# Kernel optimization log

Measured on AMD Instinct MI355X. Metric: run time of the kernel, lower is better.

The kernel has to match this reference:

```python
import jax, jax.numpy as jnp
import numpy as np

EPS = 1e-8
TEMPERATURE = 1.0


def setup_inputs() -> dict:
    key = jax.random.key(0)
    basin_seq = jax.random.normal(key, (4, 512, 64), dtype=jnp.float32)
    residual_scale = jnp.ones((), dtype=jnp.float32)  # nn.Parameter(torch.tensor(1.0))
    return {"basin_seq": basin_seq, "residual_scale": residual_scale}


def _project_to_simplex(x):
    sp = jax.nn.softplus(x)
    p = sp / (sp.sum(axis=-1, keepdims=True) + EPS)
    return jnp.maximum(p, EPS)


def _qfi_attention_weights(x, temperature):
    # x: (B, T, D)
    p = _project_to_simplex(x)
    # fisher_rao_distance_simplex re-normalizes both operands
    p = p / (p.sum(axis=-1, keepdims=True) + EPS)
    # Faithful: eps is inside the sqrt, so this is a true (B,T,T,D) reduction,
    # not sqrt(p) @ sqrt(p)^T.
    inner = jnp.sqrt(p[:, :, None, :] * p[:, None, :, :] + EPS).sum(axis=-1)  # (B,T,T)
    inner = jnp.clip(inner, -1.0 + 1e-6, 1.0 - 1e-6)
    dist = 2.0 * jnp.arccos(inner)
    logits = -dist / max(float(temperature), 1e-6)
    return jax.nn.softmax(logits, axis=-1)  # (B,T,T)


def _phi_from_activations(acts):
    # acts: (B, T, D)
    t = acts.shape[1]
    x = acts - acts.mean(axis=1, keepdims=True)
    cov = jnp.einsum('btd,bte->bde', x, x) / (t + EPS)
    var = jnp.maximum(jnp.diagonal(cov, axis1=-2, axis2=-1), EPS)  # (B,D)
    denom = jnp.maximum(jnp.sqrt(var[:, :, None] * var[:, None, :]), EPS)
    corr = jnp.clip(cov / denom, -1.0, 1.0)
    d = corr.shape[-1]
    offdiag = corr * (1.0 - jnp.eye(d, dtype=corr.dtype))
    return jnp.abs(offdiag).mean(axis=(-2, -1))  # (B,)


def _kappa_proxy(x):
    return jnp.linalg.norm(x, axis=-1).mean(axis=-1)  # (B,)


def reference(basin_seq, residual_scale):
    x = basin_seq
    for _ in range(2):
        w = _qfi_attention_weights(x, TEMPERATURE)
        x_attn = jnp.einsum('bij,bjd->bid', w, x)
        x = 0.5 * x + 0.5 * x_attn
        x = x + 0.01 * residual_scale * (x_attn - x)
    phi = _phi_from_activations(x)
    kappa = _kappa_proxy(x)
    return (x, phi, kappa)
```

## Files before the change

kernel.cpp:

```cpp
#include <hip/hip_runtime.h>
#include <math.h>

#define B_ 4
#define T_ 512
#define D_ 64
#define EPS 1e-8f

__device__ __forceinline__ float wave_sum(float v) {
#pragma unroll
  for (int m = 1; m < 64; m <<= 1) v += __shfl_xor(v, m, 64);
  return v;
}
__device__ __forceinline__ float softplus_f(float x) {
  return fmaxf(x, 0.0f) + log1pf(expf(-fabsf(x)));
}

#define DOT4(ACC, A, Bv) \
  ACC = fmaf((A).x, (Bv).x, fmaf((A).y, (Bv).y, fmaf((A).z, (Bv).z, fmaf((A).w, (Bv).w, ACC))))

__global__ __launch_bounds__(256) void proj_kernel(const float* __restrict__ x,
                                                   float* __restrict__ s) {
  int wave = threadIdx.x >> 6, lane = threadIdx.x & 63;
  int row = blockIdx.x * 4 + wave;
  float sp = softplus_f(x[row * D_ + lane]);
  float s1 = wave_sum(sp);
  float p = sp / (s1 + EPS);
  p = fmaxf(p, EPS);
  float s2 = wave_sum(p);
  s[row * D_ + lane] = sqrtf(p / (s2 + EPS));
}

__device__ __forceinline__ void stage512(const float* __restrict__ g,
                                         float* __restrict__ lds, int tid) {
#pragma unroll
  for (int h = 0; h < 2; ++h) {
    float4 v[8];
#pragma unroll
    for (int r = 0; r < 8; ++r) {
      int slot = (h * 8 + r) * 512 + tid;
      int j = slot >> 4, c4 = slot & 15;
      v[r] = *(const float4*)(g + j * 64 + ((c4 ^ ((j >> 2) & 7)) << 2));
    }
#pragma unroll
    for (int r = 0; r < 8; ++r) {
      int slot = (h * 8 + r) * 512 + tid;
      int j = slot >> 4, c4 = slot & 15;
      *(float4*)(lds + j * 64 + (c4 << 2)) = v[r];
    }
  }
}

__global__ __launch_bounds__(512) void fiter_kernel(const float* __restrict__ s_g,
                                                    const float* __restrict__ x_g,
                                                    const float* __restrict__ rsp,
                                                    float* __restrict__ xout,
                                                    float* __restrict__ sout) {
  int b = blockIdx.y, i0 = blockIdx.x * 8;
  int tid = threadIdx.x;
  int w = tid >> 6, lane = tid & 63;
  const float* sb = s_g + (size_t)b * (T_ * D_);
  const float* xb = x_g + (size_t)b * (T_ * D_);

  __shared__ __align__(16) float sx[512 * 64];
  __shared__ __align__(16) float wlds[8 * 516];
  __shared__ __align__(16) float redv[8 * 68];
  __shared__ float redM[8][8];
  __shared__ float redS[8][8];

  stage512(sb, sx, tid);
  __syncthreads();

  int i4 = lane >> 4, j16 = lane & 15;
  int ia0 = i0 + 2 * i4;
  const float* A0 = sx + ia0 * 64;
  const float* A1 = A0 + 64;
  int mA0 = (ia0 >> 2) & 7, mA1 = ((ia0 + 1) >> 2) & 7;
  const float* Bp = sx + (w * 64 + 4 * j16) * 64;
  int mB = j16 & 7;

  float acc[2][4];
#pragma unroll
  for (int r = 0; r < 2; ++r)
#pragma unroll
    for (int c = 0; c < 4; ++c) acc[r][c] = 0.f;

#pragma unroll
  for (int d4 = 0; d4 < 16; ++d4) {
    float4 a0 = *(const float4*)(A0 + ((d4 ^ mA0) << 2));
    float4 a1 = *(const float4*)(A1 + ((d4 ^ mA1) << 2));
    int ob = (d4 ^ mB) << 2;
    float4 b0 = *(const float4*)(Bp + ob);
    float4 b1 = *(const float4*)(Bp + 64 + ob);
    float4 b2 = *(const float4*)(Bp + 128 + ob);
    float4 b3 = *(const float4*)(Bp + 192 + ob);
    DOT4(acc[0][0], a0, b0); DOT4(acc[0][1], a0, b1);
    DOT4(acc[0][2], a0, b2); DOT4(acc[0][3], a0, b3);
    DOT4(acc[1][0], a1, b0); DOT4(acc[1][1], a1, b1);
    DOT4(acc[1][2], a1, b2); DOT4(acc[1][3], a1, b3);
  }

  float S[2][4];
#pragma unroll
  for (int r = 0; r < 2; ++r)
#pragma unroll
    for (int c = 0; c < 4; ++c) {
      float inner = fminf(fmaxf(acc[r][c], -1.0f + 1e-6f), 1.0f - 1e-6f);
      S[r][c] = -2.0f * acosf(inner);
    }

  float m0 = fmaxf(fmaxf(S[0][0], S[0][1]), fmaxf(S[0][2], S[0][3]));
  float m1 = fmaxf(fmaxf(S[1][0], S[1][1]), fmaxf(S[1][2], S[1][3]));
#pragma unroll
  for (int mm = 1; mm < 16; mm <<= 1) {
    m0 = fmaxf(m0, __shfl_xor(m0, mm, 64));
    m1 = fmaxf(m1, __shfl_xor(m1, mm, 64));
  }
  if (j16 == 0) { redM[2 * i4][w] = m0; redM[2 * i4 + 1][w] = m1; }
  __syncthreads();

  stage512(xb, sx, tid);

  float M0 = redM[2 * i4][0], M1 = redM[2 * i4 + 1][0];
#pragma unroll
  for (int q = 1; q < 8; ++q) {
    M0 = fmaxf(M0, redM[2 * i4][q]);
    M1 = fmaxf(M1, redM[2 * i4 + 1][q]);
  }
  float e[2][4];
  float sl0 = 0.f, sl1 = 0.f;
#pragma unroll
  for (int c = 0; c < 4; ++c) {
    e[0][c] = __expf(S[0][c] - M0); sl0 += e[0][c];
    e[1][c] = __expf(S[1][c] - M1); sl1 += e[1][c];
  }
#pragma unroll
  for (int mm = 1; mm < 16; mm <<= 1) {
    sl0 += __shfl_xor(sl0, mm, 64);
    sl1 += __shfl_xor(sl1, mm, 64);
  }
  if (j16 == 0) { redS[2 * i4][w] = sl0; redS[2 * i4 + 1][w] = sl1; }
  int wb = w * 64 + 4 * j16;
#pragma unroll
  for (int r = 0; r < 2; ++r)
#pragma unroll
    for (int c = 0; c < 4; ++c) wlds[(2 * i4 + r) * 516 + wb + c] = e[r][c];
  __syncthreads();

  int js = tid & 15, dg = (tid >> 4) & 15, ig = tid >> 8;
  int xcol = ((dg ^ (js & 7)) << 2);
  float pacc[4][4];
#pragma unroll
  for (int ii = 0; ii < 4; ++ii)
#pragma unroll
    for (int k = 0; k < 4; ++k) pacc[ii][k] = 0.f;

#pragma unroll 2
  for (int jj = 0; jj < 8; ++jj) {
    int jbase = jj * 64 + js * 4;
    const float* xr = sx + jbase * 64 + xcol;
    float4 x0 = *(const float4*)(xr);
    float4 x1 = *(const float4*)(xr + 64);
    float4 x2 = *(const float4*)(xr + 128);
    float4 x3 = *(const float4*)(xr + 192);
#pragma unroll
    for (int ii = 0; ii < 4; ++ii) {
      float4 wv = *(const float4*)(wlds + (4 * ig + ii) * 516 + jbase);
      pacc[ii][0] = fmaf(wv.x, x0.x, fmaf(wv.y, x1.x, fmaf(wv.z, x2.x, fmaf(wv.w, x3.x, pacc[ii][0]))));
      pacc[ii][1] = fmaf(wv.x, x0.y, fmaf(wv.y, x1.y, fmaf(wv.z, x2.y, fmaf(wv.w, x3.y, pacc[ii][1]))));
      pacc[ii][2] = fmaf(wv.x, x0.z, fmaf(wv.y, x1.z, fmaf(wv.z, x2.z, fmaf(wv.w, x3.z, pacc[ii][2]))));
      pacc[ii][3] = fmaf(wv.x, x0.w, fmaf(wv.y, x1.w, fmaf(wv.z, x2.w, fmaf(wv.w, x3.w, pacc[ii][3]))));
    }
  }
#pragma unroll
  for (int ii = 0; ii < 4; ++ii)
#pragma unroll
    for (int k = 0; k < 4; ++k) {
      float v = pacc[ii][k];
      v += __shfl_xor(v, 1, 64);
      v += __shfl_xor(v, 2, 64);
      v += __shfl_xor(v, 4, 64);
      v += __shfl_xor(v, 8, 64);
      pacc[ii][k] = v;
    }
  if (js == 0) {
#pragma unroll
    for (int ii = 0; ii < 4; ++ii)
      *(float4*)(redv + (4 * ig + ii) * 68 + (dg << 2)) =
          make_float4(pacc[ii][0], pacc[ii][1], pacc[ii][2], pacc[ii][3]);
  }
  __syncthreads();

  {
    int row = w, d = lane;
    float ssum = 0.f;
#pragma unroll
    for (int q = 0; q < 8; ++q) ssum += redS[row][q];
    float xa = redv[row * 68 + d] / ssum;
    int ir = i0 + row;
    int mr = (ir >> 2) & 7;
    float xv = sx[ir * 64 + (((d >> 2) ^ mr) << 2) + (d & 3)];
    float c01 = 0.01f * rsp[0];
    float xn = 0.5f * (1.0f - c01) * xv + 0.5f * (1.0f + c01) * xa;
    size_t gi = ((size_t)(b * T_) + ir) * D_ + d;
    xout[gi] = xn;
    float sp = softplus_f(xn);
    float s1 = wave_sum(sp);
    float p = sp / (s1 + EPS);
    p = fmaxf(p, EPS);
    float s2 = wave_sum(p);
    sout[gi] = sqrtf(p / (s2 + EPS));
  }
}

__global__ __launch_bounds__(256) void p1_kernel(const float* __restrict__ x,
                                                 float* __restrict__ covp,
                                                 float* __restrict__ meanp,
                                                 float* __restrict__ kappap) {
  int blk = blockIdx.x;
  int b = blk >> 5, sl = blk & 31;
  const float* xb = x + ((size_t)(b * T_) + sl * 16) * D_;
  __shared__ float tile[16][68];
  __shared__ float red2[4][64];
  __shared__ float kred[4];
  int tid = threadIdx.x;
  {
    int row = tid >> 4, c4 = tid & 15;
    *(float4*)&tile[row][c4 * 4] = *(const float4*)(xb + row * D_ + c4 * 4);
  }
  __syncthreads();

  {
    int tr = tid >> 4, qq = tid & 15;
    float ksq = 0.f;
#pragma unroll
    for (int k = 0; k < 4; ++k) {
      float v = tile[tr][qq * 4 + k];
      ksq = fmaf(v, v, ksq);
    }
    ksq += __shfl_xor(ksq, 1, 64);
    ksq += __shfl_xor(ksq, 2, 64);
    ksq += __shfl_xor(ksq, 4, 64);
    ksq += __shfl_xor(ksq, 8, 64);
    float contrib = (qq == 0) ? sqrtf(ksq) : 0.f;
    contrib = wave_sum(contrib);
    if ((tid & 63) == 0) kred[tid >> 6] = contrib;
  }

  {
    int d = tid & 63, q = tid >> 6;
    float ms = 0.f;
#pragma unroll
    for (int tt = 0; tt < 4; ++tt) ms += tile[q * 4 + tt][d];
    red2[q][d] = ms;
  }

  int dd = tid >> 2, e16 = tid & 3;
  float acc[16];
#pragma unroll
  for (int k = 0; k < 16; ++k) acc[k] = 0.f;
#pragma unroll
  for (int tt = 0; tt < 16; ++tt) {
    float xd = tile[tt][dd];
    const float4* te = (const float4*)&tile[tt][e16 * 16];
    float4 v0 = te[0], v1 = te[1], v2 = te[2], v3 = te[3];
    acc[0]  = fmaf(xd, v0.x, acc[0]);  acc[1]  = fmaf(xd, v0.y, acc[1]);
    acc[2]  = fmaf(xd, v0.z, acc[2]);  acc[3]  = fmaf(xd, v0.w, acc[3]);
    acc[4]  = fmaf(xd, v1.x, acc[4]);  acc[5]  = fmaf(xd, v1.y, acc[5]);
    acc[6]  = fmaf(xd, v1.z, acc[6]);  acc[7]  = fmaf(xd, v1.w, acc[7]);
    acc[8]  = fmaf(xd, v2.x, acc[8]);  acc[9]  = fmaf(xd, v2.y, acc[9]);
    acc[10] = fmaf(xd, v2.z, acc[10]); acc[11] = fmaf(xd, v2.w, acc[11]);
    acc[12] = fmaf(xd, v3.x, acc[12]); acc[13] = fmaf(xd, v3.y, acc[13]);
    acc[14] = fmaf(xd, v3.z, acc[14]); acc[15] = fmaf(xd, v3.w, acc[15]);
  }
  float* cp = covp + (size_t)blk * 4096 + dd * 64 + e16 * 16;
#pragma unroll
  for (int kk = 0; kk < 4; ++kk)
    *(float4*)(cp + kk * 4) =
        make_float4(acc[kk * 4], acc[kk * 4 + 1], acc[kk * 4 + 2], acc[kk * 4 + 3]);
  __syncthreads();
  if (tid < 64)
    meanp[blk * 64 + tid] = red2[0][tid] + red2[1][tid] + red2[2][tid] + red2[3][tid];
  if (tid == 0) kappap[blk] = kred[0] + kred[1] + kred[2] + kred[3];
}

__global__ __launch_bounds__(1024) void p2_kernel(const float* __restrict__ covp,
                                                  const float* __restrict__ meanp,
                                                  const float* __restrict__ kappap,
                                                  float* __restrict__ out) {
  int b = blockIdx.x;
  __shared__ float mu[64];
  __shared__ float var[64];
  __shared__ float phired[16];
  int tid = threadIdx.x;
  if (tid < 64) {
    float m = 0.f;
#pragma unroll
    for (int s = 0; s < 32; ++s) m += meanp[(b * 32 + s) * 64 + tid];
    mu[tid] = m * (1.0f / 512.0f);
  }
  __syncthreads();

  int dd = tid >> 4, e4 = tid & 15;
  float acc[4] = {0.f, 0.f, 0.f, 0.f};
#pragma unroll
  for (int s = 0; s < 32; ++s) {
    float4 v = *(const float4*)(covp + (size_t)(b * 32 + s) * 4096 + dd * 64 + e4 * 4);
    acc[0] += v.x; acc[1] += v.y; acc[2] += v.z; acc[3] += v.w;
  }
  float mud = mu[dd];
#pragma unroll
  for (int k = 0; k < 4; ++k)
    acc[k] = acc[k] * (1.0f / 512.0f) - mud * mu[e4 * 4 + k];
  if (e4 == (dd >> 2)) var[dd] = fmaxf(acc[dd & 3], EPS);
  __syncthreads();

  float vd = var[dd];
  float psum = 0.f;
#pragma unroll
  for (int k = 0; k < 4; ++k) {
    int e = e4 * 4 + k;
    if (e == dd) continue;
    float denom = fmaxf(sqrtf(vd * var[e]), EPS);
    float cc = fminf(fmaxf(acc[k] / denom, -1.0f), 1.0f);
    psum += fabsf(cc);
  }
  psum = wave_sum(psum);
  if ((tid & 63) == 0) phired[tid >> 6] = psum;
  __syncthreads();
  if (tid == 0) {
    float ph = 0.f;
#pragma unroll
    for (int q = 0; q < 16; ++q) ph += phired[q];
    out[B_ * T_ * D_ + b] = ph * (1.0f / 4096.0f);
    float ks = 0.f;
#pragma unroll
    for (int s = 0; s < 32; ++s) ks += kappap[b * 32 + s];
    out[B_ * T_ * D_ + B_ + b] = ks * (1.0f / 512.0f);
  }
}

extern "C" void kernel_launch(void* const* d_in, const int* in_sizes, int n_in,
                              void* d_out, int out_size, void* d_ws, size_t ws_size,
                              hipStream_t stream) {
  const float* x0 = (const float*)d_in[0];
  const float* rs = (const float*)d_in[1];
  float* out = (float*)d_out;
  float* s0    = (float*)d_ws;
  float* s1    = s0 + B_ * T_ * D_;
  float* x1    = s1 + B_ * T_ * D_;
  float* covp  = x1 + B_ * T_ * D_;
  float* meanp = covp + 128 * 4096;
  float* kappap = meanp + 128 * 64;

  dim3 fgrd(64, 4);
  proj_kernel<<<(B_ * T_) / 4, 256, 0, stream>>>(x0, s0);
  fiter_kernel<<<fgrd, 512, 0, stream>>>(s0, x0, rs, x1, s1);
  fiter_kernel<<<fgrd, 512, 0, stream>>>(s1, x1, rs, out, s0);
  p1_kernel<<<128, 256, 0, stream>>>(out, covp, meanp, kappap);
  p2_kernel<<<4, 1024, 0, stream>>>(covp, meanp, kappap, out);
}
```

Baseline: 96.12 us.

## Fuse simplex projection into attention kernel and merge stats kernels via last-block counter

Removes the standalone projection kernel. Each attention block now stages raw x into LDS and computes softplus-simplex-sqrt for all 512 rows of its batch in place, so the s buffers are neither written nor reread through global memory. The two covariance/phi kernels are merged into one: an atomic per-batch counter picks the last finishing block, which does the final reduction. This cuts launches from five to three, at the price of redundant transcendental work in every attention block plus threadfence/atomic overhead.

Result: slower. 173.9 us (+80.9%).

```diff
diff --git a/kernel.cpp b/kernel.cpp
--- a/kernel.cpp
+++ b/kernel.cpp
@@ -18,18 +18,6 @@
 #define DOT4(ACC, A, Bv) \
   ACC = fmaf((A).x, (Bv).x, fmaf((A).y, (Bv).y, fmaf((A).z, (Bv).z, fmaf((A).w, (Bv).w, ACC))))
 
-__global__ __launch_bounds__(256) void proj_kernel(const float* __restrict__ x,
-                                                   float* __restrict__ s) {
-  int wave = threadIdx.x >> 6, lane = threadIdx.x & 63;
-  int row = blockIdx.x * 4 + wave;
-  float sp = softplus_f(x[row * D_ + lane]);
-  float s1 = wave_sum(sp);
-  float p = sp / (s1 + EPS);
-  p = fmaxf(p, EPS);
-  float s2 = wave_sum(p);
-  s[row * D_ + lane] = sqrtf(p / (s2 + EPS));
-}
-
 __device__ __forceinline__ void stage512(const float* __restrict__ g,
                                          float* __restrict__ lds, int tid) {
 #pragma unroll
@@ -50,16 +38,17 @@
   }
 }
 
-__global__ __launch_bounds__(512) void fiter_kernel(const float* __restrict__ s_g,
-                                                    const float* __restrict__ x_g,
+template <int ZERO_CNT>
+__global__ __launch_bounds__(512) void fiter_kernel(const float* __restrict__ x_g,
                                                     const float* __restrict__ rsp,
                                                     float* __restrict__ xout,
-                                                    float* __restrict__ sout) {
+                                                    unsigned int* __restrict__ cnt) {
   int b = blockIdx.y, i0 = blockIdx.x * 8;
   int tid = threadIdx.x;
   int w = tid >> 6, lane = tid & 63;
-  const float* sb = s_g + (size_t)b * (T_ * D_);
   const float* xb = x_g + (size_t)b * (T_ * D_);
+
+  if (ZERO_CNT && blockIdx.x == 0 && blockIdx.y == 0 && tid < B_) cnt[tid] = 0u;
 
   __shared__ __align__(16) float sx[512 * 64];
   __shared__ __align__(16) float wlds[8 * 516];
@@ -67,7 +56,41 @@
   __shared__ float redM[8][8];
   __shared__ float redS[8][8];
 
-  stage512(sb, sx, tid);
+  stage512(xb, sx, tid);
+  __syncthreads();
+
+  {
+    int g = lane >> 4, d4 = lane & 15;
+#pragma unroll
+    for (int it = 0; it < 16; ++it) {
+      int r = (w << 6) + (it << 2) + g;
+      int mr = (r >> 2) & 7;
+      float* p4 = sx + r * 64 + ((d4 ^ mr) << 2);
+      float4 v = *(const float4*)p4;
+      float4 sp;
+      sp.x = softplus_f(v.x); sp.y = softplus_f(v.y);
+      sp.z = softplus_f(v.z); sp.w = softplus_f(v.w);
+      float loc = sp.x + sp.y + sp.z + sp.w;
+      loc += __shfl_xor(loc, 1, 64);
+      loc += __shfl_xor(loc, 2, 64);
+      loc += __shfl_xor(loc, 4, 64);
+      loc += __shfl_xor(loc, 8, 64);
+      float inv1 = 1.0f / (loc + EPS);
+      float4 p;
+      p.x = fmaxf(sp.x * inv1, EPS); p.y = fmaxf(sp.y * inv1, EPS);
+      p.z = fmaxf(sp.z * inv1, EPS); p.w = fmaxf(sp.w * inv1, EPS);
+      float loc2 = p.x + p.y + p.z + p.w;
+      loc2 += __shfl_xor(loc2, 1, 64);
+      loc2 += __shfl_xor(loc2, 2, 64);
+      loc2 += __shfl_xor(loc2, 4, 64);
+      loc2 += __shfl_xor(loc2, 8, 64);
+      float inv2 = 1.0f / (loc2 + EPS);
+      float4 sv;
+      sv.x = sqrtf(p.x * inv2); sv.y = sqrtf(p.y * inv2);
+      sv.z = sqrtf(p.z * inv2); sv.w = sqrtf(p.w * inv2);
+      *(float4*)p4 = sv;
+    }
+  }
   __syncthreads();
 
   int i4 = lane >> 4, j16 = lane & 15;
@@ -201,27 +224,23 @@
     float xv = sx[ir * 64 + (((d >> 2) ^ mr) << 2) + (d & 3)];
     float c01 = 0.01f * rsp[0];
     float xn = 0.5f * (1.0f - c01) * xv + 0.5f * (1.0f + c01) * xa;
-    size_t gi = ((size_t)(b * T_) + ir) * D_ + d;
-    xout[gi] = xn;
-    float sp = softplus_f(xn);
-    float s1 = wave_sum(sp);
-    float p = sp / (s1 + EPS);
-    p = fmaxf(p, EPS);
-    float s2 = wave_sum(p);
-    sout[gi] = sqrtf(p / (s2 + EPS));
-  }
-}
-
-__global__ __launch_bounds__(256) void p1_kernel(const float* __restrict__ x,
-                                                 float* __restrict__ covp,
-                                                 float* __restrict__ meanp,
-                                                 float* __restrict__ kappap) {
+    xout[((size_t)(b * T_) + ir) * D_ + d] = xn;
+  }
+}
+
+__global__ __launch_bounds__(256) void stats_kernel(const float* __restrict__ x,
+                                                    float* __restrict__ covp,
+                                                    float* __restrict__ meanp,
+                                                    float* __restrict__ kappap,
+                                                    unsigned int* __restrict__ cnt,
+                                                    float* __restrict__ out) {
   int blk = blockIdx.x;
-  int b = blk >> 5, sl = blk & 31;
-  const float* xb = x + ((size_t)(b * T_) + sl * 16) * D_;
+  int b = blk >> 5;
+  const float* xb = x + (size_t)blk * (16 * D_);
   __shared__ float tile[16][68];
   __shared__ float red2[4][64];
   __shared__ float kred[4];
+  __shared__ int lastflag;
   int tid = threadIdx.x;
   {
     int row = tid >> 4, c4 = tid & 15;
@@ -254,44 +273,49 @@
     red2[q][d] = ms;
   }
 
-  int dd = tid >> 2, e16 = tid & 3;
-  float acc[16];
-#pragma unroll
-  for (int k = 0; k < 16; ++k) acc[k] = 0.f;
-#pragma unroll
-  for (int tt = 0; tt < 16; ++tt) {
-    float xd = tile[tt][dd];
-    const float4* te = (const float4*)&tile[tt][e16 * 16];
-    float4 v0 = te[0], v1 = te[1], v2 = te[2], v3 = te[3];
-    acc[0]  = fmaf(xd, v0.x, acc[0]);  acc[1]  = fmaf(xd, v0.y, acc[1]);
-    acc[2]  = fmaf(xd, v0.z, acc[2]);  acc[3]  = fmaf(xd, v0.w, acc[3]);
-    acc[4]  = fmaf(xd, v1.x, acc[4]);  acc[5]  = fmaf(xd, v1.y, acc[5]);
-    acc[6]  = fmaf(xd, v1.z, acc[6]);  acc[7]  = fmaf(xd, v1.w, acc[7]);
-    acc[8]  = fmaf(xd, v2.x, acc[8]);  acc[9]  = fmaf(xd, v2.y, acc[9]);
-    acc[10] = fmaf(xd, v2.z, acc[10]); acc[11] = fmaf(xd, v2.w, acc[11]);
-    acc[12] = fmaf(xd, v3.x, acc[12]); acc[13] = fmaf(xd, v3.y, acc[13]);
-    acc[14] = fmaf(xd, v3.z, acc[14]); acc[15] = fmaf(xd, v3.w, acc[15]);
-  }
-  float* cp = covp + (size_t)blk * 4096 + dd * 64 + e16 * 16;
-#pragma unroll
-  for (int kk = 0; kk < 4; ++kk)
-    *(float4*)(cp + kk * 4) =
-        make_float4(acc[kk * 4], acc[kk * 4 + 1], acc[kk * 4 + 2], acc[kk * 4 + 3]);
+  {
+    int dd = tid >> 2, e16 = tid & 3;
+    float acc[16];
+#pragma unroll
+    for (int k = 0; k < 16; ++k) acc[k] = 0.f;
+#pragma unroll
+    for (int tt = 0; tt < 16; ++tt) {
+      float xd = tile[tt][dd];
+      const float4* te = (const float4*)&tile[tt][e16 * 16];
+      float4 v0 = te[0], v1 = te[1], v2 = te[2], v3 = te[3];
+      acc[0]  = fmaf(xd, v0.x, acc[0]);  acc[1]  = fmaf(xd, v0.y, acc[1]);
+      acc[2]  = fmaf(xd, v0.z, acc[2]);  acc[3]  = fmaf(xd, v0.w, acc[3]);
+      acc[4]  = fmaf(xd, v1.x, acc[4]);  acc[5]  = fmaf(xd, v1.y, acc[5]);
+      acc[6]  = fmaf(xd, v1.z, acc[6]);  acc[7]  = fmaf(xd, v1.w, acc[7]);
+      acc[8]  = fmaf(xd, v2.x, acc[8]);  acc[9]  = fmaf(xd, v2.y, acc[9]);
+      acc[10] = fmaf(xd, v2.z, acc[10]); acc[11] = fmaf(xd, v2.w, acc[11]);
+      acc[12] = fmaf(xd, v3.x, acc[12]); acc[13] = fmaf(xd, v3.y, acc[13]);
+      acc[14] = fmaf(xd, v3.z, acc[14]); acc[15] = fmaf(xd, v3.w, acc[15]);
+    }
+    float* cp = covp + (size_t)blk * 4096 + dd * 64 + e16 * 16;
+#pragma unroll
+    for (int kk = 0; kk < 4; ++kk)
+      *(float4*)(cp + kk * 4) =
+          make_float4(acc[kk * 4], acc[kk * 4 + 1], acc[kk * 4 + 2], acc[kk * 4 + 3]);
+  }
   __syncthreads();
   if (tid < 64)
     meanp[blk * 64 + tid] = red2[0][tid] + red2[1][tid] + red2[2][tid] + red2[3][tid];
   if (tid == 0) kappap[blk] = kred[0] + kred[1] + kred[2] + kred[3];
-}
-
-__global__ __launch_bounds__(1024) void p2_kernel(const float* __restrict__ covp,
-                                                  const float* __restrict__ meanp,
-                                                  const float* __restrict__ kappap,
-                                                  float* __restrict__ out) {
-  int b = blockIdx.x;
+
+  __threadfence();
+  __syncthreads();
+  if (tid == 0) {
+    unsigned int old = atomicAdd(&cnt[b], 1u);
+    lastflag = (old == 31u);
+  }
+  __syncthreads();
+  if (!lastflag) return;
+  __threadfence();
+
   __shared__ float mu[64];
   __shared__ float var[64];
-  __shared__ float phired[16];
-  int tid = threadIdx.x;
+  __shared__ float phired[4];
   if (tid < 64) {
     float m = 0.f;
 #pragma unroll
@@ -300,25 +324,32 @@
   }
   __syncthreads();
 
-  int dd = tid >> 4, e4 = tid & 15;
-  float acc[4] = {0.f, 0.f, 0.f, 0.f};
+  int dd = tid >> 2, e16 = tid & 3;
+  float acc[16];
+#pragma unroll
+  for (int k = 0; k < 16; ++k) acc[k] = 0.f;
 #pragma unroll
   for (int s = 0; s < 32; ++s) {
-    float4 v = *(const float4*)(covp + (size_t)(b * 32 + s) * 4096 + dd * 64 + e4 * 4);
-    acc[0] += v.x; acc[1] += v.y; acc[2] += v.z; acc[3] += v.w;
+    const float* cp = covp + (size_t)(b * 32 + s) * 4096 + dd * 64 + e16 * 16;
+#pragma unroll
+    for (int kk = 0; kk < 4; ++kk) {
+      float4 v = *(const float4*)(cp + kk * 4);
+      acc[kk * 4] += v.x; acc[kk * 4 + 1] += v.y;
+      acc[kk * 4 + 2] += v.z; acc[kk * 4 + 3] += v.w;
+    }
   }
   float mud = mu[dd];
 #pragma unroll
-  for (int k = 0; k < 4; ++k)
-    acc[k] = acc[k] * (1.0f / 512.0f) - mud * mu[e4 * 4 + k];
-  if (e4 == (dd >> 2)) var[dd] = fmaxf(acc[dd & 3], EPS);
+  for (int k = 0; k < 16; ++k)
+    acc[k] = acc[k] * (1.0f / 512.0f) - mud * mu[e16 * 16 + k];
+  if (e16 == (dd >> 4)) var[dd] = fmaxf(acc[dd & 15], EPS);
   __syncthreads();
 
   float vd = var[dd];
   float psum = 0.f;
 #pragma unroll
-  for (int k = 0; k < 4; ++k) {
-    int e = e4 * 4 + k;
+  for (int k = 0; k < 16; ++k) {
+    int e = e16 * 16 + k;
     if (e == dd) continue;
     float denom = fmaxf(sqrtf(vd * var[e]), EPS);
     float cc = fminf(fmaxf(acc[k] / denom, -1.0f), 1.0f);
@@ -328,10 +359,8 @@
   if ((tid & 63) == 0) phired[tid >> 6] = psum;
   __syncthreads();
   if (tid == 0) {
-    float ph = 0.f;
-#pragma unroll
-    for (int q = 0; q < 16; ++q) ph += phired[q];
-    out[B_ * T_ * D_ + b] = ph * (1.0f / 4096.0f);
+    out[B_ * T_ * D_ + b] = (phired[0] + phired[1] + phired[2] + phired[3]) *
+                            (1.0f / 4096.0f);
     float ks = 0.f;
 #pragma unroll
     for (int s = 0; s < 32; ++s) ks += kappap[b * 32 + s];
@@ -345,17 +374,14 @@
   const float* x0 = (const float*)d_in[0];
   const float* rs = (const float*)d_in[1];
   float* out = (float*)d_out;
-  float* s0    = (float*)d_ws;
-  float* s1    = s0 + B_ * T_ * D_;
-  float* x1    = s1 + B_ * T_ * D_;
+  float* x1    = (float*)d_ws;
   float* covp  = x1 + B_ * T_ * D_;
   float* meanp = covp + 128 * 4096;
   float* kappap = meanp + 128 * 64;
+  unsigned int* cnt = (unsigned int*)(kappap + 128);
 
   dim3 fgrd(64, 4);
-  proj_kernel<<<(B_ * T_) / 4, 256, 0, stream>>>(x0, s0);
-  fiter_kernel<<<fgrd, 512, 0, stream>>>(s0, x0, rs, x1, s1);
-  fiter_kernel<<<fgrd, 512, 0, stream>>>(s1, x1, rs, out, s0);
-  p1_kernel<<<128, 256, 0, stream>>>(out, covp, meanp, kappap);
-  p2_kernel<<<4, 1024, 0, stream>>>(covp, meanp, kappap, out);
-}
+  fiter_kernel<1><<<fgrd, 512, 0, stream>>>(x0, rs, x1, cnt);
+  fiter_kernel<0><<<fgrd, 512, 0, stream>>>(x1, rs, out, cnt);
+  stats_kernel<<<128, 256, 0, stream>>>(out, covp, meanp, kappap, cnt, out);
+}
```

## Fuse all five kernels into one cooperative kernel with grid syncs

Applied to the files above, without the earlier changes.

Merges the projection, both attention iterations, and the two covariance/phi/kappa reduction stages into a single cooperative launch of 256 blocks. Grid-wide syncs replace the kernel boundaries. This removes four launch gaps and their tail effects. In exchange, the final reduction stages run inside 512-thread blocks with only 128 or 4 active blocks, and every block still carries about 150KB of LDS, so occupancy stays at one block per CU. The second iteration also skips writing the unused simplex output.

Measured after the change: 209.0 us. +117.5%, slower.

```diff
diff --git a/kernel.cpp b/kernel.cpp
--- a/kernel.cpp
+++ b/kernel.cpp
@@ -1,5 +1,8 @@
 #include <hip/hip_runtime.h>
+#include <hip/hip_cooperative_groups.h>
 #include <math.h>
+
+namespace cg = cooperative_groups;
 
 #define B_ 4
 #define T_ 512
@@ -18,18 +21,6 @@
 #define DOT4(ACC, A, Bv) \
   ACC = fmaf((A).x, (Bv).x, fmaf((A).y, (Bv).y, fmaf((A).z, (Bv).z, fmaf((A).w, (Bv).w, ACC))))
 
-__global__ __launch_bounds__(256) void proj_kernel(const float* __restrict__ x,
-                                                   float* __restrict__ s) {
-  int wave = threadIdx.x >> 6, lane = threadIdx.x & 63;
-  int row = blockIdx.x * 4 + wave;
-  float sp = softplus_f(x[row * D_ + lane]);
-  float s1 = wave_sum(sp);
-  float p = sp / (s1 + EPS);
-  p = fmaxf(p, EPS);
-  float s2 = wave_sum(p);
-  s[row * D_ + lane] = sqrtf(p / (s2 + EPS));
-}
-
 __device__ __forceinline__ void stage512(const float* __restrict__ g,
                                          float* __restrict__ lds, int tid) {
 #pragma unroll
@@ -50,22 +41,13 @@
   }
 }
 
-__global__ __launch_bounds__(512) void fiter_kernel(const float* __restrict__ s_g,
-                                                    const float* __restrict__ x_g,
-                                                    const float* __restrict__ rsp,
-                                                    float* __restrict__ xout,
-                                                    float* __restrict__ sout) {
-  int b = blockIdx.y, i0 = blockIdx.x * 8;
-  int tid = threadIdx.x;
+__device__ __forceinline__ void fiter_body(
+    const float* __restrict__ sb, const float* __restrict__ xb,
+    float* __restrict__ xoutb, float* __restrict__ soutb, int i0, int tid,
+    float c01, float* __restrict__ sx, float* __restrict__ wlds,
+    float* __restrict__ redv, float* __restrict__ redM,
+    float* __restrict__ redS, int write_s) {
   int w = tid >> 6, lane = tid & 63;
-  const float* sb = s_g + (size_t)b * (T_ * D_);
-  const float* xb = x_g + (size_t)b * (T_ * D_);
-
-  __shared__ __align__(16) float sx[512 * 64];
-  __shared__ __align__(16) float wlds[8 * 516];
-  __shared__ __align__(16) float redv[8 * 68];
-  __shared__ float redM[8][8];
-  __shared__ float redS[8][8];
 
   stage512(sb, sx, tid);
   __syncthreads();
@@ -115,16 +97,16 @@
     m0 = fmaxf(m0, __shfl_xor(m0, mm, 64));
     m1 = fmaxf(m1, __shfl_xor(m1, mm, 64));
   }
-  if (j16 == 0) { redM[2 * i4][w] = m0; redM[2 * i4 + 1][w] = m1; }
+  if (j16 == 0) { redM[(2 * i4) * 8 + w] = m0; redM[(2 * i4 + 1) * 8 + w] = m1; }
   __syncthreads();
 
   stage512(xb, sx, tid);
 
-  float M0 = redM[2 * i4][0], M1 = redM[2 * i4 + 1][0];
+  float M0 = redM[(2 * i4) * 8], M1 = redM[(2 * i4 + 1) * 8];
 #pragma unroll
   for (int q = 1; q < 8; ++q) {
-    M0 = fmaxf(M0, redM[2 * i4][q]);
-    M1 = fmaxf(M1, redM[2 * i4 + 1][q]);
+    M0 = fmaxf(M0, redM[(2 * i4) * 8 + q]);
+    M1 = fmaxf(M1, redM[(2 * i4 + 1) * 8 + q]);
   }
   float e[2][4];
   float sl0 = 0.f, sl1 = 0.f;
@@ -138,7 +120,7 @@
     sl0 += __shfl_xor(sl0, mm, 64);
     sl1 += __shfl_xor(sl1, mm, 64);
   }
-  if (j16 == 0) { redS[2 * i4][w] = sl0; redS[2 * i4 + 1][w] = sl1; }
+  if (j16 == 0) { redS[(2 * i4) * 8 + w] = sl0; redS[(2 * i4 + 1) * 8 + w] = sl1; }
   int wb = w * 64 + 4 * j16;
 #pragma unroll
   for (int r = 0; r < 2; ++r)
@@ -194,148 +176,177 @@
     int row = w, d = lane;
     float ssum = 0.f;
 #pragma unroll
-    for (int q = 0; q < 8; ++q) ssum += redS[row][q];
+    for (int q = 0; q < 8; ++q) ssum += redS[row * 8 + q];
     float xa = redv[row * 68 + d] / ssum;
     int ir = i0 + row;
     int mr = (ir >> 2) & 7;
     float xv = sx[ir * 64 + (((d >> 2) ^ mr) << 2) + (d & 3)];
-    float c01 = 0.01f * rsp[0];
     float xn = 0.5f * (1.0f - c01) * xv + 0.5f * (1.0f + c01) * xa;
-    size_t gi = ((size_t)(b * T_) + ir) * D_ + d;
-    xout[gi] = xn;
-    float sp = softplus_f(xn);
-    float s1 = wave_sum(sp);
-    float p = sp / (s1 + EPS);
+    xoutb[ir * 64 + d] = xn;
+    if (write_s) {
+      float sp = softplus_f(xn);
+      float s1 = wave_sum(sp);
+      float p = sp / (s1 + EPS);
+      p = fmaxf(p, EPS);
+      float s2 = wave_sum(p);
+      soutb[ir * 64 + d] = sqrtf(p / (s2 + EPS));
+    }
+  }
+}
+
+__global__ __launch_bounds__(512) void mega_kernel(
+    const float* __restrict__ x0, const float* __restrict__ rsp,
+    float* __restrict__ out, float* __restrict__ s0, float* __restrict__ x1,
+    float* __restrict__ s1, float* __restrict__ covp,
+    float* __restrict__ meanp, float* __restrict__ kappap) {
+  cg::grid_group grid = cg::this_grid();
+  int bid = blockIdx.x, tid = threadIdx.x;
+  int w = tid >> 6, lane = tid & 63;
+
+  __shared__ __align__(16) float sx[512 * 64];
+  __shared__ __align__(16) float wlds[8 * 516];
+  __shared__ __align__(16) float redv[8 * 68];
+  __shared__ float redM[64];
+  __shared__ float redS[64];
+
+  {
+    int row = bid * 8 + w;
+    float sp = softplus_f(x0[row * 64 + lane]);
+    float s1v = wave_sum(sp);
+    float p = sp / (s1v + EPS);
     p = fmaxf(p, EPS);
-    float s2 = wave_sum(p);
-    sout[gi] = sqrtf(p / (s2 + EPS));
-  }
-}
-
-__global__ __launch_bounds__(256) void p1_kernel(const float* __restrict__ x,
-                                                 float* __restrict__ covp,
-                                                 float* __restrict__ meanp,
-                                                 float* __restrict__ kappap) {
-  int blk = blockIdx.x;
-  int b = blk >> 5, sl = blk & 31;
-  const float* xb = x + ((size_t)(b * T_) + sl * 16) * D_;
-  __shared__ float tile[16][68];
-  __shared__ float red2[4][64];
-  __shared__ float kred[4];
-  int tid = threadIdx.x;
-  {
-    int row = tid >> 4, c4 = tid & 15;
-    *(float4*)&tile[row][c4 * 4] = *(const float4*)(xb + row * D_ + c4 * 4);
-  }
-  __syncthreads();
-
-  {
-    int tr = tid >> 4, qq = tid & 15;
-    float ksq = 0.f;
-#pragma unroll
-    for (int k = 0; k < 4; ++k) {
-      float v = tile[tr][qq * 4 + k];
-      ksq = fmaf(v, v, ksq);
-    }
-    ksq += __shfl_xor(ksq, 1, 64);
-    ksq += __shfl_xor(ksq, 2, 64);
-    ksq += __shfl_xor(ksq, 4, 64);
-    ksq += __shfl_xor(ksq, 8, 64);
-    float contrib = (qq == 0) ? sqrtf(ksq) : 0.f;
-    contrib = wave_sum(contrib);
-    if ((tid & 63) == 0) kred[tid >> 6] = contrib;
-  }
-
-  {
-    int d = tid & 63, q = tid >> 6;
-    float ms = 0.f;
-#pragma unroll
-    for (int tt = 0; tt < 4; ++tt) ms += tile[q * 4 + tt][d];
-    red2[q][d] = ms;
-  }
-
-  int dd = tid >> 2, e16 = tid & 3;
-  float acc[16];
-#pragma unroll
-  for (int k = 0; k < 16; ++k) acc[k] = 0.f;
-#pragma unroll
-  for (int tt = 0; tt < 16; ++tt) {
-    float xd = tile[tt][dd];
-    const float4* te = (const float4*)&tile[tt][e16 * 16];
-    float4 v0 = te[0], v1 = te[1], v2 = te[2], v3 = te[3];
-    acc[0]  = fmaf(xd, v0.x, acc[0]);  acc[1]  = fmaf(xd, v0.y, acc[1]);
-    acc[2]  = fmaf(xd, v0.z, acc[2]);  acc[3]  = fmaf(xd, v0.w, acc[3]);
-    acc[4]  = fmaf(xd, v1.x, acc[4]);  acc[5]  = fmaf(xd, v1.y, acc[5]);
-    acc[6]  = fmaf(xd, v1.z, acc[6]);  acc[7]  = fmaf(xd, v1.w, acc[7]);
-    acc[8]  = fmaf(xd, v2.x, acc[8]);  acc[9]  = fmaf(xd, v2.y, acc[9]);
-    acc[10] = fmaf(xd, v2.z, acc[10]); acc[11] = fmaf(xd, v2.w, acc[11]);
-    acc[12] = fmaf(xd, v3.x, acc[12]); acc[13] = fmaf(xd, v3.y, acc[13]);
-    acc[14] = fmaf(xd, v3.z, acc[14]); acc[15] = fmaf(xd, v3.w, acc[15]);
-  }
-  float* cp = covp + (size_t)blk * 4096 + dd * 64 + e16 * 16;
-#pragma unroll
-  for (int kk = 0; kk < 4; ++kk)
-    *(float4*)(cp + kk * 4) =
-        make_float4(acc[kk * 4], acc[kk * 4 + 1], acc[kk * 4 + 2], acc[kk * 4 + 3]);
-  __syncthreads();
-  if (tid < 64)
-    meanp[blk * 64 + tid] = red2[0][tid] + red2[1][tid] + red2[2][tid] + red2[3][tid];
-  if (tid == 0) kappap[blk] = kred[0] + kred[1] + kred[2] + kred[3];
-}
-
-__global__ __launch_bounds__(1024) void p2_kernel(const float* __restrict__ covp,
-                                                  const float* __restrict__ meanp,
-                                                  const float* __restrict__ kappap,
-                                                  float* __restrict__ out) {
-  int b = blockIdx.x;
-  __shared__ float mu[64];
-  __shared__ float var[64];
-  __shared__ float phired[16];
-  int tid = threadIdx.x;
-  if (tid < 64) {
-    float m = 0.f;
-#pragma unroll
-    for (int s = 0; s < 32; ++s) m += meanp[(b * 32 + s) * 64 + tid];
-    mu[tid] = m * (1.0f / 512.0f);
-  }
-  __syncthreads();
-
-  int dd = tid >> 4, e4 = tid & 15;
-  float acc[4] = {0.f, 0.f, 0.f, 0.f};
-#pragma unroll
-  for (int s = 0; s < 32; ++s) {
-    float4 v = *(const float4*)(covp + (size_t)(b * 32 + s) * 4096 + dd * 64 + e4 * 4);
-    acc[0] += v.x; acc[1] += v.y; acc[2] += v.z; acc[3] += v.w;
-  }
-  float mud = mu[dd];
-#pragma unroll
-  for (int k = 0; k < 4; ++k)
-    acc[k] = acc[k] * (1.0f / 512.0f) - mud * mu[e4 * 4 + k];
-  if (e4 == (dd >> 2)) var[dd] = fmaxf(acc[dd & 3], EPS);
-  __syncthreads();
-
-  float vd = var[dd];
-  float psum = 0.f;
-#pragma unroll
-  for (int k = 0; k < 4; ++k) {
-    int e = e4 * 4 + k;
-    if (e == dd) continue;
-    float denom = fmaxf(sqrtf(vd * var[e]), EPS);
-    float cc = fminf(fmaxf(acc[k] / denom, -1.0f), 1.0f);
-    psum += fabsf(cc);
-  }
-  psum = wave_sum(psum);
-  if ((tid & 63) == 0) phired[tid >> 6] = psum;
-  __syncthreads();
-  if (tid == 0) {
-    float ph = 0.f;
-#pragma unroll
-    for (int q = 0; q < 16; ++q) ph += phired[q];
-    out[B_ * T_ * D_ + b] = ph * (1.0f / 4096.0f);
-    float ks = 0.f;
-#pragma unroll
-    for (int s = 0; s < 32; ++s) ks += kappap[b * 32 + s];
-    out[B_ * T_ * D_ + B_ + b] = ks * (1.0f / 512.0f);
+    float s2v = wave_sum(p);
+    s0[row * 64 + lane] = sqrtf(p / (s2v + EPS));
+  }
+  grid.sync();
+
+  float c01 = 0.01f * rsp[0];
+  int b = bid >> 6, i0 = (bid & 63) * 8;
+  size_t boff = (size_t)b * (T_ * D_);
+
+  fiter_body(s0 + boff, x0 + boff, x1 + boff, s1 + boff, i0, tid, c01, sx,
+             wlds, redv, redM, redS, 1);
+  grid.sync();
+
+  fiter_body(s1 + boff, x1 + boff, out + boff, (float*)0, i0, tid, c01, sx,
+             wlds, redv, redM, redS, 0);
+  grid.sync();
+
+  float* tile = sx;
+  float* red2 = sx + 1152;
+  float* kred = sx + 1408;
+  float* mu = sx + 1472;
+  float* var = sx + 1536;
+  float* phired = sx + 1600;
+  if (bid < 128) {
+    const float* xb = out + (size_t)bid * (16 * D_);
+    if (tid < 256) {
+      int row = tid >> 4, c4 = tid & 15;
+      *(float4*)&tile[row * 68 + c4 * 4] = *(const float4*)(xb + row * 64 + c4 * 4);
+    }
+    __syncthreads();
+
+    if (tid < 256) {
+      int tr = tid >> 4, qq = tid & 15;
+      float ksq = 0.f;
+#pragma unroll
+      for (int k = 0; k < 4; ++k) {
+        float v = tile[tr * 68 + qq * 4 + k];
+        ksq = fmaf(v, v, ksq);
+      }
+      ksq += __shfl_xor(ksq, 1, 64);
+      ksq += __shfl_xor(ksq, 2, 64);
+      ksq += __shfl_xor(ksq, 4, 64);
+      ksq += __shfl_xor(ksq, 8, 64);
+      float contrib = (qq == 0) ? sqrtf(ksq) : 0.f;
+      contrib = wave_sum(contrib);
+      if ((tid & 63) == 0) kred[tid >> 6] = contrib;
+      int d = tid & 63, q = tid >> 6;
+      float ms = 0.f;
+#pragma unroll
+      for (int tt = 0; tt < 4; ++tt) ms += tile[(q * 4 + tt) * 68 + d];
+      red2[q * 64 + d] = ms;
+    }
+
+    {
+      int dd = tid >> 3, e8 = tid & 7;
+      float acc[8];
+#pragma unroll
+      for (int k = 0; k < 8; ++k) acc[k] = 0.f;
+#pragma unroll
+      for (int tt = 0; tt < 16; ++tt) {
+        float xd = tile[tt * 68 + dd];
+        float4 v0 = *(const float4*)&tile[tt * 68 + e8 * 8];
+        float4 v1 = *(const float4*)&tile[tt * 68 + e8 * 8 + 4];
+        acc[0] = fmaf(xd, v0.x, acc[0]); acc[1] = fmaf(xd, v0.y, acc[1]);
+        acc[2] = fmaf(xd, v0.z, acc[2]); acc[3] = fmaf(xd, v0.w, acc[3]);
+        acc[4] = fmaf(xd, v1.x, acc[4]); acc[5] = fmaf(xd, v1.y, acc[5]);
+        acc[6] = fmaf(xd, v1.z, acc[6]); acc[7] = fmaf(xd, v1.w, acc[7]);
+      }
+      float* cp = covp + (size_t)bid * 4096 + dd * 64 + e8 * 8;
+      *(float4*)(cp) = make_float4(acc[0], acc[1], acc[2], acc[3]);
+      *(float4*)(cp + 4) = make_float4(acc[4], acc[5], acc[6], acc[7]);
+    }
+    __syncthreads();
+    if (tid < 64)
+      meanp[bid * 64 + tid] =
+          red2[tid] + red2[64 + tid] + red2[128 + tid] + red2[192 + tid];
+    if (tid == 0) kappap[bid] = kred[0] + kred[1] + kred[2] + kred[3];
+  }
+  grid.sync();
+
+  if (bid < B_) {
+    int bb = bid;
+    if (tid < 64) {
+      float m = 0.f;
+#pragma unroll
+      for (int s = 0; s < 32; ++s) m += meanp[(bb * 32 + s) * 64 + tid];
+      mu[tid] = m * (1.0f / 512.0f);
+    }
+    __syncthreads();
+
+    int dd = tid >> 3, e8 = tid & 7;
+    float acc[8];
+#pragma unroll
+    for (int k = 0; k < 8; ++k) acc[k] = 0.f;
+#pragma unroll
+    for (int s = 0; s < 32; ++s) {
+      const float* cp = covp + (size_t)(bb * 32 + s) * 4096 + dd * 64 + e8 * 8;
+      float4 v0 = *(const float4*)(cp);
+      float4 v1 = *(const float4*)(cp + 4);
+      acc[0] += v0.x; acc[1] += v0.y; acc[2] += v0.z; acc[3] += v0.w;
+      acc[4] += v1.x; acc[5] += v1.y; acc[6] += v1.z; acc[7] += v1.w;
+    }
+    float mud = mu[dd];
+#pragma unroll
+    for (int k = 0; k < 8; ++k)
+      acc[k] = acc[k] * (1.0f / 512.0f) - mud * mu[e8 * 8 + k];
+    if (e8 == (dd >> 3)) var[dd] = fmaxf(acc[dd & 7], EPS);
+    __syncthreads();
+
+    float vd = var[dd];
+    float psum = 0.f;
+#pragma unroll
+    for (int k = 0; k < 8; ++k) {
+      int e = e8 * 8 + k;
+      if (e == dd) continue;
+      float denom = fmaxf(sqrtf(vd * var[e]), EPS);
+      float cc = fminf(fmaxf(acc[k] / denom, -1.0f), 1.0f);
+      psum += fabsf(cc);
+    }
+    psum = wave_sum(psum);
+    if ((tid & 63) == 0) phired[tid >> 6] = psum;
+    __syncthreads();
+    if (tid == 0) {
+      float ph = 0.f;
+#pragma unroll
+      for (int q = 0; q < 8; ++q) ph += phired[q];
+      out[B_ * T_ * D_ + bb] = ph * (1.0f / 4096.0f);
+      float ks = 0.f;
+#pragma unroll
+      for (int s = 0; s < 32; ++s) ks += kappap[bb * 32 + s];
+      out[B_ * T_ * D_ + B_ + bb] = ks * (1.0f / 512.0f);
+    }
   }
 }
 
@@ -345,17 +356,16 @@
   const float* x0 = (const float*)d_in[0];
   const float* rs = (const float*)d_in[1];
   float* out = (float*)d_out;
-  float* s0    = (float*)d_ws;
-  float* s1    = s0 + B_ * T_ * D_;
-  float* x1    = s1 + B_ * T_ * D_;
-  float* covp  = x1 + B_ * T_ * D_;
+  float* s0 = (float*)d_ws;
+  float* x1 = s0 + B_ * T_ * D_;
+  float* s1 = x1 + B_ * T_ * D_;
+  float* covp = s1 + B_ * T_ * D_;
   float* meanp = covp + 128 * 4096;
   float* kappap = meanp + 128 * 64;
 
-  dim3 fgrd(64, 4);
-  proj_kernel<<<(B_ * T_) / 4, 256, 0, stream>>>(x0, s0);
-  fiter_kernel<<<fgrd, 512, 0, stream>>>(s0, x0, rs, x1, s1);
-  fiter_kernel<<<fgrd, 512, 0, stream>>>(s1, x1, rs, out, s0);
-  p1_kernel<<<128, 256, 0, stream>>>(out, covp, meanp, kappap);
-  p2_kernel<<<4, 1024, 0, stream>>>(covp, meanp, kappap, out);
-}
+  void* args[] = {(void*)&x0,   (void*)&rs,    (void*)&out,
+                  (void*)&s0,   (void*)&x1,    (void*)&s1,
+                  (void*)&covp, (void*)&meanp, (void*)&kappap};
+  hipLaunchCooperativeKernel((const void*)mega_kernel, dim3(256), dim3(512),
+                             args, 0, stream);
+}
```

## Fuse covariance/kappa partials into second attention iteration and drop p1 kernel

Applied to the files above, without the earlier changes.

The separate p1 covariance-partial kernel is folded into the second fiter_kernel pass through a template flag. Each block computes the 8x64 outer-product partials, column sums and row norms from its freshly produced rows, which removes one launch and a re-read of x. The second pass also skips writing the unused simplex projection. In exchange, partial buffers double to 256 blocks, so the finalize kernel reads twice as much covariance data, and the fused kernel uses more LDS.

Result: slower. 99.76 us (+3.8%).

```diff
diff --git a/kernel.cpp b/kernel.cpp
--- a/kernel.cpp
+++ b/kernel.cpp
@@ -50,11 +50,12 @@
   }
 }
 
-__global__ __launch_bounds__(512) void fiter_kernel(const float* __restrict__ s_g,
-                                                    const float* __restrict__ x_g,
-                                                    const float* __restrict__ rsp,
-                                                    float* __restrict__ xout,
-                                                    float* __restrict__ sout) {
+template <int WRITE_S, int DO_COV>
+__global__ __launch_bounds__(512) void fiter_kernel(
+    const float* __restrict__ s_g, const float* __restrict__ x_g,
+    const float* __restrict__ rsp, float* __restrict__ xout,
+    float* __restrict__ sout, float* __restrict__ covp,
+    float* __restrict__ meanp, float* __restrict__ kappap) {
   int b = blockIdx.y, i0 = blockIdx.x * 8;
   int tid = threadIdx.x;
   int w = tid >> 6, lane = tid & 63;
@@ -66,6 +67,8 @@
   __shared__ __align__(16) float redv[8 * 68];
   __shared__ float redM[8][8];
   __shared__ float redS[8][8];
+  __shared__ float t8[8][68];
+  __shared__ float kred8[8];
 
   stage512(sb, sx, tid);
   __syncthreads();
@@ -203,99 +206,67 @@
     float xn = 0.5f * (1.0f - c01) * xv + 0.5f * (1.0f + c01) * xa;
     size_t gi = ((size_t)(b * T_) + ir) * D_ + d;
     xout[gi] = xn;
-    float sp = softplus_f(xn);
-    float s1 = wave_sum(sp);
-    float p = sp / (s1 + EPS);
-    p = fmaxf(p, EPS);
-    float s2 = wave_sum(p);
-    sout[gi] = sqrtf(p / (s2 + EPS));
-  }
-}
-
-__global__ __launch_bounds__(256) void p1_kernel(const float* __restrict__ x,
-                                                 float* __restrict__ covp,
-                                                 float* __restrict__ meanp,
-                                                 float* __restrict__ kappap) {
-  int blk = blockIdx.x;
-  int b = blk >> 5, sl = blk & 31;
-  const float* xb = x + ((size_t)(b * T_) + sl * 16) * D_;
-  __shared__ float tile[16][68];
-  __shared__ float red2[4][64];
-  __shared__ float kred[4];
-  int tid = threadIdx.x;
-  {
-    int row = tid >> 4, c4 = tid & 15;
-    *(float4*)&tile[row][c4 * 4] = *(const float4*)(xb + row * D_ + c4 * 4);
-  }
-  __syncthreads();
-
-  {
-    int tr = tid >> 4, qq = tid & 15;
-    float ksq = 0.f;
-#pragma unroll
-    for (int k = 0; k < 4; ++k) {
-      float v = tile[tr][qq * 4 + k];
-      ksq = fmaf(v, v, ksq);
-    }
-    ksq += __shfl_xor(ksq, 1, 64);
-    ksq += __shfl_xor(ksq, 2, 64);
-    ksq += __shfl_xor(ksq, 4, 64);
-    ksq += __shfl_xor(ksq, 8, 64);
-    float contrib = (qq == 0) ? sqrtf(ksq) : 0.f;
-    contrib = wave_sum(contrib);
-    if ((tid & 63) == 0) kred[tid >> 6] = contrib;
-  }
-
-  {
-    int d = tid & 63, q = tid >> 6;
-    float ms = 0.f;
-#pragma unroll
-    for (int tt = 0; tt < 4; ++tt) ms += tile[q * 4 + tt][d];
-    red2[q][d] = ms;
-  }
-
-  int dd = tid >> 2, e16 = tid & 3;
-  float acc[16];
-#pragma unroll
-  for (int k = 0; k < 16; ++k) acc[k] = 0.f;
-#pragma unroll
-  for (int tt = 0; tt < 16; ++tt) {
-    float xd = tile[tt][dd];
-    const float4* te = (const float4*)&tile[tt][e16 * 16];
-    float4 v0 = te[0], v1 = te[1], v2 = te[2], v3 = te[3];
-    acc[0]  = fmaf(xd, v0.x, acc[0]);  acc[1]  = fmaf(xd, v0.y, acc[1]);
-    acc[2]  = fmaf(xd, v0.z, acc[2]);  acc[3]  = fmaf(xd, v0.w, acc[3]);
-    acc[4]  = fmaf(xd, v1.x, acc[4]);  acc[5]  = fmaf(xd, v1.y, acc[5]);
-    acc[6]  = fmaf(xd, v1.z, acc[6]);  acc[7]  = fmaf(xd, v1.w, acc[7]);
-    acc[8]  = fmaf(xd, v2.x, acc[8]);  acc[9]  = fmaf(xd, v2.y, acc[9]);
-    acc[10] = fmaf(xd, v2.z, acc[10]); acc[11] = fmaf(xd, v2.w, acc[11]);
-    acc[12] = fmaf(xd, v3.x, acc[12]); acc[13] = fmaf(xd, v3.y, acc[13]);
-    acc[14] = fmaf(xd, v3.z, acc[14]); acc[15] = fmaf(xd, v3.w, acc[15]);
-  }
-  float* cp = covp + (size_t)blk * 4096 + dd * 64 + e16 * 16;
-#pragma unroll
-  for (int kk = 0; kk < 4; ++kk)
-    *(float4*)(cp + kk * 4) =
-        make_float4(acc[kk * 4], acc[kk * 4 + 1], acc[kk * 4 + 2], acc[kk * 4 + 3]);
-  __syncthreads();
-  if (tid < 64)
-    meanp[blk * 64 + tid] = red2[0][tid] + red2[1][tid] + red2[2][tid] + red2[3][tid];
-  if (tid == 0) kappap[blk] = kred[0] + kred[1] + kred[2] + kred[3];
-}
-
-__global__ __launch_bounds__(1024) void p2_kernel(const float* __restrict__ covp,
-                                                  const float* __restrict__ meanp,
-                                                  const float* __restrict__ kappap,
-                                                  float* __restrict__ out) {
-  int b = blockIdx.x;
+    if (WRITE_S) {
+      float sp = softplus_f(xn);
+      float s1 = wave_sum(sp);
+      float p = sp / (s1 + EPS);
+      p = fmaxf(p, EPS);
+      float s2 = wave_sum(p);
+      sout[gi] = sqrtf(p / (s2 + EPS));
+    }
+    if (DO_COV) {
+      t8[row][d] = xn;
+      float ksq = wave_sum(xn * xn);
+      if (lane == 0) kred8[row] = sqrtf(ksq);
+    }
+  }
+
+  if (DO_COV) {
+    __syncthreads();
+    int blk = b * 64 + blockIdx.x;
+    int dd = tid >> 3, e8 = tid & 7;
+    float ca[8];
+#pragma unroll
+    for (int k = 0; k < 8; ++k) ca[k] = 0.f;
+#pragma unroll
+    for (int r = 0; r < 8; ++r) {
+      float xd = t8[r][dd];
+      float4 v0 = *(const float4*)&t8[r][e8 * 8];
+      float4 v1 = *(const float4*)&t8[r][e8 * 8 + 4];
+      ca[0] = fmaf(xd, v0.x, ca[0]); ca[1] = fmaf(xd, v0.y, ca[1]);
+      ca[2] = fmaf(xd, v0.z, ca[2]); ca[3] = fmaf(xd, v0.w, ca[3]);
+      ca[4] = fmaf(xd, v1.x, ca[4]); ca[5] = fmaf(xd, v1.y, ca[5]);
+      ca[6] = fmaf(xd, v1.z, ca[6]); ca[7] = fmaf(xd, v1.w, ca[7]);
+    }
+    float* cp = covp + (size_t)blk * 4096 + dd * 64 + e8 * 8;
+    *(float4*)(cp) = make_float4(ca[0], ca[1], ca[2], ca[3]);
+    *(float4*)(cp + 4) = make_float4(ca[4], ca[5], ca[6], ca[7]);
+    if (tid < 64) {
+      float ms = 0.f;
+#pragma unroll
+      for (int r = 0; r < 8; ++r) ms += t8[r][tid];
+      meanp[blk * 64 + tid] = ms;
+    }
+    if (tid == 0) {
+      float ks = 0.f;
+#pragma unroll
+      for (int r = 0; r < 8; ++r) ks += kred8[r];
+      kappap[blk] = ks;
+    }
+  }
+}
+
+__global__ __launch_bounds__(1024) void finalize_kernel(
+    const float* __restrict__ covp, const float* __restrict__ meanp,
+    const float* __restrict__ kappap, float* __restrict__ out) {
+  int b = blockIdx.x, tid = threadIdx.x;
   __shared__ float mu[64];
   __shared__ float var[64];
   __shared__ float phired[16];
-  int tid = threadIdx.x;
   if (tid < 64) {
     float m = 0.f;
 #pragma unroll
-    for (int s = 0; s < 32; ++s) m += meanp[(b * 32 + s) * 64 + tid];
+    for (int s = 0; s < 64; ++s) m += meanp[(b * 64 + s) * 64 + tid];
     mu[tid] = m * (1.0f / 512.0f);
   }
   __syncthreads();
@@ -303,8 +274,8 @@
   int dd = tid >> 4, e4 = tid & 15;
   float acc[4] = {0.f, 0.f, 0.f, 0.f};
 #pragma unroll
-  for (int s = 0; s < 32; ++s) {
-    float4 v = *(const float4*)(covp + (size_t)(b * 32 + s) * 4096 + dd * 64 + e4 * 4);
+  for (int s = 0; s < 64; ++s) {
+    float4 v = *(const float4*)(covp + (size_t)(b * 64 + s) * 4096 + dd * 64 + e4 * 4);
     acc[0] += v.x; acc[1] += v.y; acc[2] += v.z; acc[3] += v.w;
   }
   float mud = mu[dd];
@@ -334,7 +305,7 @@
     out[B_ * T_ * D_ + b] = ph * (1.0f / 4096.0f);
     float ks = 0.f;
 #pragma unroll
-    for (int s = 0; s < 32; ++s) ks += kappap[b * 32 + s];
+    for (int s = 0; s < 64; ++s) ks += kappap[b * 64 + s];
     out[B_ * T_ * D_ + B_ + b] = ks * (1.0f / 512.0f);
   }
 }
@@ -349,13 +320,14 @@
   float* s1    = s0 + B_ * T_ * D_;
   float* x1    = s1 + B_ * T_ * D_;
   float* covp  = x1 + B_ * T_ * D_;
-  float* meanp = covp + 128 * 4096;
-  float* kappap = meanp + 128 * 64;
+  float* meanp = covp + 256 * 4096;
+  float* kappap = meanp + 256 * 64;
 
   dim3 fgrd(64, 4);
   proj_kernel<<<(B_ * T_) / 4, 256, 0, stream>>>(x0, s0);
-  fiter_kernel<<<fgrd, 512, 0, stream>>>(s0, x0, rs, x1, s1);
-  fiter_kernel<<<fgrd, 512, 0, stream>>>(s1, x1, rs, out, s0);
-  p1_kernel<<<128, 256, 0, stream>>>(out, covp, meanp, kappap);
-  p2_kernel<<<4, 1024, 0, stream>>>(covp, meanp, kappap, out);
-}
+  fiter_kernel<1, 0><<<fgrd, 512, 0, stream>>>(s0, x0, rs, x1, s1, (float*)0,
+                                               (float*)0, (float*)0);
+  fiter_kernel<0, 1><<<fgrd, 512, 0, stream>>>(s1, x1, rs, out, (float*)0, covp,
+                                               meanp, kappap);
+  finalize_kernel<<<4, 1024, 0, stream>>>(covp, meanp, kappap, out);
+}
```
